# Kernel tuning notes

Hardware: AMD Instinct MI355X
Metric: run time of the kernel (lower is better)

## Reference

```python
import jax, jax.numpy as jnp
import numpy as np

NF = 64        # feature channels (nf == inter_channels == in_channels)
BURST = 14     # burst_size from Args
H = 128
W = 128
SCALE = 0.02   # weight init scale keeps softmax logits in a sane range


def conv1x1(x, w, b):
    # x: [B,C,H,W], w: [O,C], b: [O]
    return jnp.einsum('bchw,oc->bohw', x, w) + b[None, :, None, None]


def setup_inputs() -> dict:
    key = jax.random.key(0)
    ks = jax.random.split(key, 32)
    inp = {'aligned_fea': jax.random.normal(ks[0], (BURST, NF, H, W), dtype=jnp.float32)}
    names = ['gc', 'thc', 'phc', 'Wc', 'gh', 'thh', 'phh', 'Wh', 'gw', 'thw', 'phw', 'Ww']
    for i, n in enumerate(names):
        inp[n + '_w'] = SCALE * jax.random.normal(ks[1 + 2 * i], (NF, NF), dtype=jnp.float32)
        inp[n + '_b'] = SCALE * jax.random.normal(ks[2 + 2 * i], (NF,), dtype=jnp.float32)
    inp['fus_w'] = SCALE * jax.random.normal(ks[26], (NF, BURST * NF * 3), dtype=jnp.float32)
    inp['fus_b'] = SCALE * jax.random.normal(ks[27], (NF,), dtype=jnp.float32)
    return inp


def _forward(aligned_fea,
             gc_w, gc_b, thc_w, thc_b, phc_w, phc_b, Wc_w, Wc_b,
             gh_w, gh_b, thh_w, thh_b, phh_w, phh_b, Wh_w, Wh_b,
             gw_w, gw_b, thw_w, thw_b, phw_w, phw_b, Ww_w, Ww_b,
             fus_w, fus_b):
    B, C, h, w = aligned_fea.shape  # [14, 64, 128, 128]
    x = aligned_fea
    ref = aligned_fea[0:1]  # [1,C,H,W]

    # ---- channel non-local (self) ----
    g = conv1x1(x, gc_w, gc_b).reshape(B, C, h * w)
    th = conv1x1(x, thc_w, thc_b).reshape(B, C, h * w)
    ph = conv1x1(x, phc_w, phc_b).reshape(B, C, h * w)
    f = jnp.einsum('bcn,bdn->bcd', th, ph)            # [B,C,C]
    f = jax.nn.softmax(f, axis=1)                     # softmax over dim=1 as in torch
    y = jnp.einsum('bcd,bdn->bcn', f, g)              # [B,C,HW]
    y = jnp.transpose(y, (0, 2, 1)).reshape(B, C, h, w)  # permute+view as in torch
    zc = conv1x1(y, Wc_w, Wc_b) + x

    # ---- height non-local (cross with ref) ----
    g = conv1x1(x, gh_w, gh_b).reshape(B, h, C * w)
    th = conv1x1(ref, thh_w, thh_b).reshape(1, h, C * w)
    ph = conv1x1(x, phh_w, phh_b).reshape(B, h, C * w)
    f = jnp.einsum('bik,bjk->bij', jnp.broadcast_to(th, (B, h, C * w)), ph)  # [B,H,H]
    f = jax.nn.softmax(f, axis=1)
    y = jnp.einsum('bij,bjk->bik', f, g)              # [B,H,C*W]
    y = jnp.transpose(y, (0, 2, 1)).reshape(B, C, h, w)  # requires H == W
    zh = conv1x1(y, Wh_w, Wh_b) + x

    # ---- width non-local (cross with ref) ----
    g = conv1x1(x, gw_w, gw_b).reshape(B, w, C * h)
    th = conv1x1(ref, thw_w, thw_b).reshape(1, w, C * h)
    ph = conv1x1(x, phw_w, phw_b).reshape(B, w, C * h)
    f = jnp.einsum('bik,bjk->bij', jnp.broadcast_to(th, (B, w, C * h)), ph)  # [B,W,W]
    f = jax.nn.softmax(f, axis=1)
    y = jnp.einsum('bij,bjk->bik', f, g)              # [B,W,C*H]
    y = jnp.transpose(y, (0, 2, 1)).reshape(B, C, h, w)
    zw = conv1x1(y, Ww_w, Ww_b) + x

    # ---- fusion: cat frames along channel in order [c, h, w] ----
    feat = jnp.concatenate([zc.reshape(1, B * C, h, w),
                            zh.reshape(1, B * C, h, w),
                            zw.reshape(1, B * C, h, w)], axis=1)  # [1, 3*B*C, H, W]
    out = conv1x1(feat, fus_w, fus_b)
    return jnp.where(out >= 0, out, 0.2 * out)  # LeakyReLU(0.2)


def reference(aligned_fea,
              gc_w, gc_b, thc_w, thc_b, phc_w, phc_b, Wc_w, Wc_b,
              gh_w, gh_b, thh_w, thh_b, phh_w, phh_b, Wh_w, Wh_b,
              gw_w, gw_b, thw_w, thw_b, phw_w, phw_b, Ww_w, Ww_b,
              fus_w, fus_b):
    return _forward(aligned_fea,
                    gc_w, gc_b, thc_w, thc_b, phc_w, phc_b, Wc_w, Wc_b,
                    gh_w, gh_b, thh_w, thh_b, phh_w, phh_b, Wh_w, Wh_b,
                    gw_w, gw_b, thw_w, thw_b, phw_w, phw_b, Ww_w, Ww_b,
                    fus_w, fus_b)
```

## Files before the change

kernel.cpp:

```cpp
#include <hip/hip_runtime.h>

#define NF 64
#define BURST 14
#define NPIX 16384
#define CN (NF * NPIX)
#define LP 72

typedef short bf16x8 __attribute__((ext_vector_type(8)));
typedef float f32x4 __attribute__((ext_vector_type(4)));
typedef unsigned short us4 __attribute__((ext_vector_type(4)));

__device__ inline unsigned short f2bf(float f) {
    unsigned int u = __float_as_uint(f);
    return (unsigned short)((u + 0x7fffu + ((u >> 16) & 1u)) >> 16);
}
__device__ inline float bf2f(unsigned short u) {
    return __uint_as_float(((unsigned int)u) << 16);
}

__global__ __launch_bounds__(256) void cast_x(const float* __restrict__ X,
                                              unsigned short* __restrict__ XB,
                                              unsigned short* __restrict__ XT,
                                              float* __restrict__ S)
{
    __shared__ unsigned short Xs[128][LP];
    __shared__ float red[256];
    const int tid = threadIdx.x;
    const int p0 = blockIdx.x * 128;
    const int b = blockIdx.y;
    const size_t boff = (size_t)b * CN;
#pragma unroll
    for (int i = 0; i < 8; ++i) {
        const int id = tid + 256 * i;
        const int c = id >> 5, p4 = (id & 31) * 4;
        float4 v = *(const float4*)&X[boff + (size_t)c * NPIX + p0 + p4];
        us4 r;
        r.x = f2bf(v.x); r.y = f2bf(v.y); r.z = f2bf(v.z); r.w = f2bf(v.w);
        *(us4*)&XB[boff + (size_t)c * NPIX + p0 + p4] = r;
        Xs[p4 + 0][c] = r.x; Xs[p4 + 1][c] = r.y;
        Xs[p4 + 2][c] = r.z; Xs[p4 + 3][c] = r.w;
    }
    __syncthreads();
#pragma unroll
    for (int i = 0; i < 4; ++i) {
        const int id = tid + 256 * i;
        const int row = id >> 3, c8 = (id & 7) * 8;
        *(bf16x8*)&XT[boff + (size_t)(p0 + row) * 64 + c8] = *(const bf16x8*)&Xs[row][c8];
    }
    {
        const int c = tid & 63, qq = tid >> 6;
        float sv = 0.f;
        for (int pp = qq * 32; pp < qq * 32 + 32; ++pp) sv += bf2f(Xs[pp][c]);
        red[tid] = sv;
        __syncthreads();
        if (tid < 64) {
            const float t = red[tid] + red[64 + tid] + red[128 + tid] + red[192 + tid];
            atomicAdd(&S[(b * 2 + (p0 >= 8192 ? 1 : 0)) * 64 + tid], t);
        }
    }
}

__global__ __launch_bounds__(256) void precompute(
    const float* __restrict__ fus_w, const float* __restrict__ fus_b,
    const float* __restrict__ Wc, const float* __restrict__ bWc,
    const float* __restrict__ Wh, const float* __restrict__ bWh,
    const float* __restrict__ Ww, const float* __restrict__ bWw,
    const float* __restrict__ gcw, const float* __restrict__ ghw,
    const float* __restrict__ gww,
    unsigned short* __restrict__ M16, unsigned short* __restrict__ Wc16,
    float* __restrict__ cb, unsigned short* __restrict__ gT16)
{
    const int blk = blockIdx.x, tid = threadIdx.x;
    if (blk < 42) {
        __shared__ float Fl[64][65];
        __shared__ float Wl[64][65];
        const int g = blk / 14, b = blk % 14;
        const float* Wg = (g == 0) ? Wc : (g == 1) ? Wh : Ww;
#pragma unroll
        for (int i = 0; i < 4; ++i) {
            const int id = tid + 256 * i;
            const int r = id >> 4, c4 = (id & 15) * 4;
            float4 v = *(const float4*)&fus_w[r * 2688 + g * 896 + b * 64 + c4];
            Fl[r][c4] = v.x; Fl[r][c4 + 1] = v.y; Fl[r][c4 + 2] = v.z; Fl[r][c4 + 3] = v.w;
            float4 u = *(const float4*)&Wg[r * 64 + c4];
            Wl[r][c4] = u.x; Wl[r][c4 + 1] = u.y; Wl[r][c4 + 2] = u.z; Wl[r][c4 + 3] = u.w;
        }
        __syncthreads();
        const int o = tid & 63, qq = tid >> 6;
        float s[16];
#pragma unroll
        for (int i = 0; i < 16; ++i) s[i] = 0.f;
        for (int c2 = 0; c2 < 64; ++c2) {
            const float fv = Fl[o][c2];
#pragma unroll
            for (int i = 0; i < 16; ++i) s[i] += fv * Wl[c2][qq * 16 + i];
        }
        unsigned short* Mout = M16 + (size_t)blk * 4096;
#pragma unroll
        for (int i = 0; i < 16; i += 4) {
            us4 r4; r4.x = f2bf(s[i]); r4.y = f2bf(s[i + 1]); r4.z = f2bf(s[i + 2]); r4.w = f2bf(s[i + 3]);
            *(us4*)&Mout[o * 64 + qq * 16 + i] = r4;
        }
    } else if (blk < 98) {
        const int e0 = (blk - 42) * 1024 + tid * 4;
        const int o = e0 / 896, bc = e0 - o * 896;
        float4 a = *(const float4*)&fus_w[o * 2688 + bc];
        float4 b2 = *(const float4*)&fus_w[o * 2688 + 896 + bc];
        float4 c3 = *(const float4*)&fus_w[o * 2688 + 1792 + bc];
        us4 r;
        r.x = f2bf(a.x + b2.x + c3.x); r.y = f2bf(a.y + b2.y + c3.y);
        r.z = f2bf(a.z + b2.z + c3.z); r.w = f2bf(a.w + b2.w + c3.w);
        *(us4*)&Wc16[e0] = r;
    } else if (blk < 106) {
        __shared__ float red[256];
        const int o = (blk - 98) * 8 + (tid >> 5);
        const int lane = tid & 31;
        float s = 0.f;
        for (int t = 0; t < 84; ++t) {
            const int ch = lane + 32 * t;
            const int g = ch / 896, c2 = ch & 63;
            const float bg = (g == 0) ? bWc[c2] : (g == 1) ? bWh[c2] : bWw[c2];
            s += fus_w[o * 2688 + ch] * bg;
        }
        red[tid] = s;
        __syncthreads();
        if (tid < 8) {
            const int oo = (blk - 98) * 8 + tid;
            float t = fus_b[oo];
            for (int i = 0; i < 32; ++i) t += red[tid * 32 + i];
            cb[oo] = t;
        }
    } else {
        const int g = blk - 106;
        const float* wg = (g == 0) ? gcw : (g == 1) ? ghw : gww;
        unsigned short* dst = gT16 + (size_t)g * 4096;
        for (int e = tid; e < 4096; e += 256) {
            const int cp = e >> 6, d = e & 63;
            dst[e] = f2bf(wg[d * 64 + cp]);
        }
    }
}

__global__ __launch_bounds__(256) void gram(
    const unsigned short* __restrict__ XB, float* __restrict__ Gpart)
{
    const int tid = threadIdx.x;
    const int w = tid >> 6, l = tid & 63, lm = l & 15, q = l >> 4;
    const int b = blockIdx.y;
    const int mo = (w & 1) * 32, no = (w >> 1) * 32;
    const unsigned short* P = XB;
    const unsigned short* Q = XB + (size_t)b * CN;
    f32x4 a0[2][2] = {}, a1[2][2] = {}, a2[2][2] = {}, a3[2][2] = {}, a4[2][2] = {};
#pragma unroll 2
    for (int ki = 0; ki < 8; ++ki) {
        const int k = blockIdx.x * 256 + ki * 32 + q * 8;
        bf16x8 p0[2], p1[2], qm0[2], qm1[2], qn0[2], qn1[2];
#pragma unroll
        for (int mi = 0; mi < 2; ++mi) {
            const size_t rm = (size_t)(mo + mi * 16 + lm) * NPIX;
            const size_t rn = (size_t)(no + mi * 16 + lm) * NPIX;
            p0[mi]  = *(const bf16x8*)&P[rm + k];
            p1[mi]  = *(const bf16x8*)&P[rm + 8192 + k];
            qm0[mi] = *(const bf16x8*)&Q[rm + k];
            qm1[mi] = *(const bf16x8*)&Q[rm + 8192 + k];
            qn0[mi] = *(const bf16x8*)&Q[rn + k];
            qn1[mi] = *(const bf16x8*)&Q[rn + 8192 + k];
        }
#pragma unroll
        for (int mi = 0; mi < 2; ++mi)
#pragma unroll
            for (int ni = 0; ni < 2; ++ni) {
                a0[mi][ni] = __builtin_amdgcn_mfma_f32_16x16x32_bf16(qm0[mi], qn0[ni], a0[mi][ni], 0, 0, 0);
                a0[mi][ni] = __builtin_amdgcn_mfma_f32_16x16x32_bf16(qm1[mi], qn1[ni], a0[mi][ni], 0, 0, 0);
                a1[mi][ni] = __builtin_amdgcn_mfma_f32_16x16x32_bf16(p0[mi], qn0[ni], a1[mi][ni], 0, 0, 0);
                a2[mi][ni] = __builtin_amdgcn_mfma_f32_16x16x32_bf16(p0[mi], qn1[ni], a2[mi][ni], 0, 0, 0);
                a3[mi][ni] = __builtin_amdgcn_mfma_f32_16x16x32_bf16(p1[mi], qn0[ni], a3[mi][ni], 0, 0, 0);
                a4[mi][ni] = __builtin_amdgcn_mfma_f32_16x16x32_bf16(p1[mi], qn1[ni], a4[mi][ni], 0, 0, 0);
            }
    }
    float* Gp = Gpart + (size_t)(blockIdx.x * 14 + b) * 5 * 4096;
#define STORE_Z(zidx, ACC)                                                     \
    for (int mi = 0; mi < 2; ++mi)                                             \
        for (int r = 0; r < 4; ++r)                                            \
            for (int ni = 0; ni < 2; ++ni)                                     \
                Gp[zidx * 4096 + (mo + mi * 16 + q * 4 + r) * 64 + no + ni * 16 + lm] = ACC[mi][ni][r];
    STORE_Z(0, a0) STORE_Z(1, a1) STORE_Z(2, a2) STORE_Z(3, a3) STORE_Z(4, a4)
#undef STORE_Z
}

__global__ __launch_bounds__(256) void gram_reduce(
    const float* __restrict__ Gpart, float* __restrict__ G)
{
    const int e = blockIdx.x * 256 + threadIdx.x;
    float s = 0.f;
#pragma unroll
    for (int ks = 0; ks < 32; ++ks) s += Gpart[(size_t)ks * 286720 + e];
    G[e] = s;
}

__global__ __launch_bounds__(256) void sandwich(
    const float* __restrict__ thc_w, const float* __restrict__ phc_w,
    const float* __restrict__ thc_b, const float* __restrict__ phc_b,
    const float* __restrict__ thh_w, const float* __restrict__ phh_w,
    const float* __restrict__ thh_b, const float* __restrict__ phh_b,
    const float* __restrict__ thw_w, const float* __restrict__ phw_w,
    const float* __restrict__ thw_b, const float* __restrict__ phw_b,
    const float* __restrict__ G, const float* __restrict__ S,
    float* __restrict__ f1, float* __restrict__ f2)
{
    __shared__ float Wt[64][65], Wp[64][65], Gl[64][65], Tl[64][65];
    __shared__ float sth[64], sph[64], uu[64], vv[64], btl[64], bpl[64];
    const int b = blockIdx.x, y = blockIdx.y, tid = threadIdx.x;
    const float *Wth_g, *Wph_g, *bth_g, *bph_g, *Gp;
    float* outp; int dl = 0, dp = 0; float Kn;
    if (y == 0) {
        Wth_g = thc_w; Wph_g = phc_w; bth_g = thc_b; bph_g = phc_b;
        Gp = G + (size_t)(b * 5) * 4096; Kn = 16384.f;
        outp = f1 + (size_t)b * 4096;
    } else {
        const int part = (y - 1) / 4, e = (y - 1) & 3;
        dl = e >> 1; dp = e & 1;
        if (part == 0) { Wth_g = thh_w; Wph_g = phh_w; bth_g = thh_b; bph_g = phh_b; }
        else           { Wth_g = thw_w; Wph_g = phw_w; bth_g = thw_b; bph_g = phw_b; }
        Gp = G + (size_t)(b * 5 + 1 + e) * 4096; Kn = 8192.f;
        outp = f2 + (size_t)(part * 14 + b) * 16384;
    }
#pragma unroll
    for (int i = 0; i < 4; ++i) {
        const int id = tid + 256 * i;
        const int r = id >> 4, c4 = (id & 15) * 4;
        float4 v = *(const float4*)&Wth_g[r * 64 + c4];
        Wt[r][c4] = v.x; Wt[r][c4 + 1] = v.y; Wt[r][c4 + 2] = v.z; Wt[r][c4 + 3] = v.w;
        float4 u = *(const float4*)&Wph_g[r * 64 + c4];
        Wp[r][c4] = u.x; Wp[r][c4 + 1] = u.y; Wp[r][c4 + 2] = u.z; Wp[r][c4 + 3] = u.w;
        float4 g = *(const float4*)&Gp[r * 64 + c4];
        Gl[r][c4] = g.x; Gl[r][c4 + 1] = g.y; Gl[r][c4 + 2] = g.z; Gl[r][c4 + 3] = g.w;
    }
    if (tid < 64) {
        if (y == 0) { const float sf = S[b * 128 + tid] + S[b * 128 + 64 + tid]; sth[tid] = sf; sph[tid] = sf; }
        else { sth[tid] = S[dl * 64 + tid]; sph[tid] = S[b * 128 + dp * 64 + tid]; }
        btl[tid] = bth_g[tid]; bpl[tid] = bph_g[tid];
    }
    __syncthreads();
    if (tid < 64) {
        float su = 0.f, sv = 0.f;
        for (int c = 0; c < 64; ++c) { su += Wt[tid][c] * sth[c]; sv += Wp[tid][c] * sph[c]; }
        uu[tid] = su; vv[tid] = sv;
    }
    const int t = tid & 63, qq = tid >> 6;
    float r16[16];
#pragma unroll
    for (int i = 0; i < 16; ++i) r16[i] = 0.f;
    for (int c = 0; c < 64; ++c) {
        const float fv = Wt[t][c];
#pragma unroll
        for (int i = 0; i < 16; ++i) r16[i] += fv * Gl[c][qq * 16 + i];
    }
#pragma unroll
    for (int i = 0; i < 16; ++i) Tl[t][qq * 16 + i] = r16[i];
    __syncthreads();
#pragma unroll
    for (int i = 0; i < 16; ++i) r16[i] = 0.f;
    for (int c = 0; c < 64; ++c) {
        const float tv = Tl[t][c];
#pragma unroll
        for (int i = 0; i < 16; ++i) r16[i] += tv * Wp[qq * 16 + i][c];
    }
    if (y == 0) {
#pragma unroll
        for (int i = 0; i < 16; ++i) {
            const int d = qq * 16 + i;
            outp[t * 64 + d] = r16[i] + uu[t] * bpl[d] + btl[t] * vv[d] + Kn * btl[t] * bpl[d];
        }
    } else {
#pragma unroll
        for (int i = 0; i < 16; ++i) {
            const int tp = qq * 16 + i;
            outp[(2 * t + dl) * 128 + 2 * tp + dp] =
                r16[i] + uu[t] * bpl[tp] + btl[t] * vv[tp] + Kn * btl[t] * bpl[tp];
        }
    }
}

__global__ __launch_bounds__(256) void softmax_all(
    const float* __restrict__ f1, const float* __restrict__ f2,
    const float* __restrict__ gcb, const float* __restrict__ ghb,
    const float* __restrict__ gwb,
    unsigned short* __restrict__ o1, unsigned short* __restrict__ o2d,
    float* __restrict__ B1, float* __restrict__ B2)
{
    __shared__ float red[256];
    __shared__ float mxA[128], invA[128];
    __shared__ float bgl[64];
    const int bx = blockIdx.x, tid = threadIdx.x;
    if (bx < 14) {
        const float* Fb = f1 + (size_t)bx * 4096;
        unsigned short* Ob = o1 + (size_t)bx * 4096;
        if (tid < 64) bgl[tid] = gcb[tid];
        const int d = tid & 63, qq = tid >> 6;
        float mx = -1e30f;
        for (int c = qq * 16; c < qq * 16 + 16; ++c) mx = fmaxf(mx, Fb[c * 64 + d]);
        red[tid] = mx;
        __syncthreads();
        if (tid < 64) mxA[tid] = fmaxf(fmaxf(red[tid], red[64 + tid]), fmaxf(red[128 + tid], red[192 + tid]));
        __syncthreads();
        const float m = mxA[d];
        float s = 0.f;
        for (int c = qq * 16; c < qq * 16 + 16; ++c) s += __expf(Fb[c * 64 + d] - m);
        red[tid] = s;
        __syncthreads();
        if (tid < 64) invA[tid] = 1.f / (red[tid] + red[64 + tid] + red[128 + tid] + red[192 + tid]);
        __syncthreads();
        const int e0 = tid * 16;
        const int d0 = e0 & 63;
        float bp = 0.f;
#pragma unroll
        for (int i = 0; i < 16; i += 4) {
            us4 r4;
            float v0 = __expf(Fb[e0 + i] - mxA[d0 + i]) * invA[d0 + i];
            float v1 = __expf(Fb[e0 + i + 1] - mxA[d0 + i + 1]) * invA[d0 + i + 1];
            float v2 = __expf(Fb[e0 + i + 2] - mxA[d0 + i + 2]) * invA[d0 + i + 2];
            float v3 = __expf(Fb[e0 + i + 3] - mxA[d0 + i + 3]) * invA[d0 + i + 3];
            bp += v0 * bgl[d0 + i] + v1 * bgl[d0 + i + 1] + v2 * bgl[d0 + i + 2] + v3 * bgl[d0 + i + 3];
            r4.x = f2bf(v0); r4.y = f2bf(v1); r4.z = f2bf(v2); r4.w = f2bf(v3);
            *(us4*)&Ob[e0 + i] = r4;
        }
        red[tid] = bp;
        __syncthreads();
        if (tid < 64)
            B1[bx * 64 + tid] = red[tid * 4] + red[tid * 4 + 1] + red[tid * 4 + 2] + red[tid * 4 + 3];
    } else {
        const int idx = bx - 14;
        const float* Fb = f2 + (size_t)idx * 16384;
        if (tid < 64) bgl[tid] = (idx < 14) ? ghb[tid] : gwb[tid];
        const int j = tid & 127, ih = tid >> 7;
        float mx = -1e30f;
        for (int i = ih * 64; i < ih * 64 + 64; ++i) mx = fmaxf(mx, Fb[i * 128 + j]);
        red[tid] = mx;
        __syncthreads();
        if (tid < 128) mxA[tid] = fmaxf(red[tid], red[128 + tid]);
        __syncthreads();
        const float m = mxA[j];
        float s = 0.f;
        for (int i = ih * 64; i < ih * 64 + 64; ++i) s += __expf(Fb[i * 128 + j] - m);
        red[tid] = s;
        __syncthreads();
        if (tid < 128) invA[tid] = 1.f / (red[tid] + red[128 + tid]);
        __syncthreads();
        const int e0 = tid * 64;
        const int irow = tid >> 1;
        const int j0 = e0 & 127;
        unsigned short vt[2][32];
        float bp = 0.f;
        for (int ii = 0; ii < 64; ++ii) {
            const int jj = j0 + ii;
            const float v = __expf(Fb[e0 + ii] - mxA[jj]) * invA[jj];
            bp += v * bgl[jj >> 1];
            vt[jj & 1][ii >> 1] = f2bf(v);
        }
        unsigned short* Od = o2d + (size_t)idx * 16384 + irow * 64 + (j0 >> 1);
#pragma unroll
        for (int dlt = 0; dlt < 2; ++dlt)
#pragma unroll
            for (int ss = 0; ss < 32; ss += 4)
                *(us4*)&Od[dlt * 8192 + ss] = *(us4*)&vt[dlt][ss];
        red[tid] = bp;
        __syncthreads();
        if (tid < 128) B2[idx * 128 + tid] = red[2 * tid] + red[2 * tid + 1];
    }
}

__global__ __launch_bounds__(256) void kmat(
    const unsigned short* __restrict__ f16_1, const unsigned short* __restrict__ f2d,
    const unsigned short* __restrict__ gT16,
    unsigned short* __restrict__ K1, unsigned short* __restrict__ K2)
{
    const int b = blockIdx.x, y = blockIdx.y, tid = threadIdx.x;
    const int w = tid >> 6, l = tid & 63, lm = l & 15, q = l >> 4;
    if (y == 0) {
        const unsigned short* A = f16_1 + (size_t)b * 4096;
        const unsigned short* Bm = gT16;
        const int mo = (w & 1) * 32, no = (w >> 1) * 32;
        f32x4 acc[2][2] = {};
#pragma unroll
        for (int ks = 0; ks < 2; ++ks) {
            const int k = ks * 32 + q * 8;
            bf16x8 a[2], bb[2];
#pragma unroll
            for (int mi = 0; mi < 2; ++mi) a[mi] = *(const bf16x8*)&A[(mo + mi * 16 + lm) * 64 + k];
#pragma unroll
            for (int ni = 0; ni < 2; ++ni) bb[ni] = *(const bf16x8*)&Bm[(no + ni * 16 + lm) * 64 + k];
#pragma unroll
            for (int mi = 0; mi < 2; ++mi)
#pragma unroll
                for (int ni = 0; ni < 2; ++ni)
                    acc[mi][ni] = __builtin_amdgcn_mfma_f32_16x16x32_bf16(a[mi], bb[ni], acc[mi][ni], 0, 0, 0);
        }
        unsigned short* Kp = K1 + (size_t)b * 4096;
#pragma unroll
        for (int mi = 0; mi < 2; ++mi)
#pragma unroll
            for (int r = 0; r < 4; ++r)
#pragma unroll
                for (int ni = 0; ni < 2; ++ni)
                    Kp[(mo + mi * 16 + q * 4 + r) * 64 + no + ni * 16 + lm] = f2bf(acc[mi][ni][r]);
    } else {
        const int part = y - 1;
        const unsigned short* Bm = gT16 + (size_t)(1 + part) * 4096;
        unsigned short* Kp = K2 + (size_t)(part * 14 + b) * 16384;
        for (int dlt = 0; dlt < 2; ++dlt) {
            const unsigned short* A = f2d + (size_t)(part * 14 + b) * 16384 + dlt * 8192;
            const int mo = (w & 1) * 64, no = (w >> 1) * 32;
            f32x4 acc[4][2] = {};
#pragma unroll
            for (int ks = 0; ks < 2; ++ks) {
                const int k = ks * 32 + q * 8;
                bf16x8 a[4], bb[2];
#pragma unroll
                for (int mi = 0; mi < 4; ++mi) a[mi] = *(const bf16x8*)&A[(mo + mi * 16 + lm) * 64 + k];
#pragma unroll
                for (int ni = 0; ni < 2; ++ni) bb[ni] = *(const bf16x8*)&Bm[(no + ni * 16 + lm) * 64 + k];
#pragma unroll
                for (int mi = 0; mi < 4; ++mi)
#pragma unroll
                    for (int ni = 0; ni < 2; ++ni)
                        acc[mi][ni] = __builtin_amdgcn_mfma_f32_16x16x32_bf16(a[mi], bb[ni], acc[mi][ni], 0, 0, 0);
            }
#pragma unroll
            for (int mi = 0; mi < 4; ++mi)
#pragma unroll
                for (int r = 0; r < 4; ++r)
#pragma unroll
                    for (int ni = 0; ni < 2; ++ni)
                        Kp[dlt * 8192 + (mo + mi * 16 + q * 4 + r) * 64 + no + ni * 16 + lm] = f2bf(acc[mi][ni][r]);
        }
    }
}

__global__ __launch_bounds__(256) void fold_res(
    const unsigned short* __restrict__ Wcomb, const unsigned short* __restrict__ XT,
    float* __restrict__ Out)
{
    const int tid = threadIdx.x;
    const int w = tid >> 6, l = tid & 63, lm = l & 15, q = l >> 4;
    const int p0 = blockIdx.x * 64 + (w >> 1) * 32;
    const int oh = (w & 1) * 32;
    f32x4 acc[2][2] = {};
    for (int b = 0; b < 14; ++b) {
#pragma unroll
        for (int ks = 0; ks < 2; ++ks) {
            const int c0 = ks * 32 + q * 8;
            bf16x8 a[2], bb[2];
#pragma unroll
            for (int mi = 0; mi < 2; ++mi)
                a[mi] = *(const bf16x8*)&Wcomb[(oh + mi * 16 + lm) * 896 + b * 64 + c0];
#pragma unroll
            for (int ni = 0; ni < 2; ++ni)
                bb[ni] = *(const bf16x8*)&XT[(size_t)b * CN + (size_t)(p0 + ni * 16 + lm) * 64 + c0];
#pragma unroll
            for (int mi = 0; mi < 2; ++mi)
#pragma unroll
                for (int ni = 0; ni < 2; ++ni)
                    acc[mi][ni] = __builtin_amdgcn_mfma_f32_16x16x32_bf16(a[mi], bb[ni], acc[mi][ni], 0, 0, 0);
        }
    }
#pragma unroll
    for (int mi = 0; mi < 2; ++mi)
#pragma unroll
        for (int r = 0; r < 4; ++r) {
            const int o = oh + mi * 16 + q * 4 + r;
#pragma unroll
            for (int ni = 0; ni < 2; ++ni)
                Out[(size_t)o * NPIX + p0 + ni * 16 + lm] = acc[mi][ni][r];
        }
}

__global__ __launch_bounds__(256) void pv1k(
    const unsigned short* __restrict__ XT, const unsigned short* __restrict__ K1,
    const float* __restrict__ B1, unsigned short* __restrict__ Y)
{
    const int tid = threadIdx.x;
    const int w = tid >> 6, l = tid & 63, lm = l & 15, q = l >> 4;
    const int b = blockIdx.z;
    const int p0 = blockIdx.x * 256 + w * 64;
    const unsigned short* Xb = XT + (size_t)b * CN;
    const unsigned short* Kb = K1 + (size_t)b * 4096;
    f32x4 acc[4][4] = {};
#pragma unroll
    for (int ks = 0; ks < 2; ++ks) {
        const int c0 = ks * 32 + q * 8;
        bf16x8 a[4], bb[4];
#pragma unroll
        for (int mi = 0; mi < 4; ++mi) a[mi] = *(const bf16x8*)&Xb[(size_t)(p0 + mi * 16 + lm) * 64 + c0];
#pragma unroll
        for (int ni = 0; ni < 4; ++ni) bb[ni] = *(const bf16x8*)&Kb[(ni * 16 + lm) * 64 + c0];
#pragma unroll
        for (int mi = 0; mi < 4; ++mi)
#pragma unroll
            for (int ni = 0; ni < 4; ++ni)
                acc[mi][ni] = __builtin_amdgcn_mfma_f32_16x16x32_bf16(a[mi], bb[ni], acc[mi][ni], 0, 0, 0);
    }
    unsigned short* Yb = Y + (size_t)b * CN;
#pragma unroll
    for (int mi = 0; mi < 4; ++mi)
#pragma unroll
        for (int r = 0; r < 4; ++r) {
            const int p = p0 + mi * 16 + q * 4 + r;
#pragma unroll
            for (int ni = 0; ni < 4; ++ni) {
                const int c = ni * 16 + lm;
                Yb[(size_t)p * 64 + c] = f2bf(acc[mi][ni][r] + B1[b * 64 + c]);
            }
        }
}

__global__ __launch_bounds__(256) void pv23k(
    const unsigned short* __restrict__ XT, const unsigned short* __restrict__ K2,
    const float* __restrict__ B2, unsigned short* __restrict__ Y2,
    unsigned short* __restrict__ Y3)
{
    const int tid = threadIdx.x;
    const int w = tid >> 6, l = tid & 63, lm = l & 15, q = l >> 4;
    const int part = blockIdx.z / 14, b = blockIdx.z % 14;
    const int k00 = blockIdx.x * 256 + w * 64;
    const int i0 = blockIdx.y * 64;
    const unsigned short* Xb = XT + (size_t)b * CN;
    const unsigned short* Kb = K2 + (size_t)(part * 14 + b) * 16384;
    const float* Bb = B2 + (part * 14 + b) * 128;
    f32x4 acc[4][4] = {};
#pragma unroll
    for (int dlt = 0; dlt < 2; ++dlt) {
#pragma unroll
        for (int ks = 0; ks < 2; ++ks) {
            const int c0 = ks * 32 + q * 8;
            bf16x8 a[4], bb[4];
#pragma unroll
            for (int mi = 0; mi < 4; ++mi)
                a[mi] = *(const bf16x8*)&Xb[(size_t)(dlt * 8192 + k00 + mi * 16 + lm) * 64 + c0];
#pragma unroll
            for (int ni = 0; ni < 4; ++ni)
                bb[ni] = *(const bf16x8*)&Kb[dlt * 8192 + (i0 + ni * 16 + lm) * 64 + c0];
#pragma unroll
            for (int mi = 0; mi < 4; ++mi)
#pragma unroll
                for (int ni = 0; ni < 4; ++ni)
                    acc[mi][ni] = __builtin_amdgcn_mfma_f32_16x16x32_bf16(a[mi], bb[ni], acc[mi][ni], 0, 0, 0);
        }
    }
    unsigned short* Yb = (part ? Y3 : Y2) + (size_t)b * CN;
#pragma unroll
    for (int mi = 0; mi < 4; ++mi)
#pragma unroll
        for (int r = 0; r < 4; ++r) {
            const int k = k00 + mi * 16 + q * 4 + r;
#pragma unroll
            for (int ni = 0; ni < 4; ++ni) {
                const int ii = i0 + ni * 16 + lm;
                Yb[(size_t)k * 128 + ii] = f2bf(acc[mi][ni][r] + Bb[ii]);
            }
        }
}

__global__ __launch_bounds__(256) void yfold(
    const unsigned short* __restrict__ M16,
    const unsigned short* __restrict__ Y1, const unsigned short* __restrict__ Y2,
    const unsigned short* __restrict__ Y3, float* __restrict__ Out)
{
    __shared__ unsigned short As[64][LP];
    __shared__ unsigned short Ss[128][LP];
    const int tid = threadIdx.x;
    const int z = blockIdx.z;
    const unsigned short* Ap = M16 + (size_t)z * 14 * 4096;
    const unsigned short* S = (z == 0) ? Y1 : (z == 1) ? Y2 : Y3;
    const int p0 = blockIdx.x * 128;
    const int t0 = blockIdx.y * 7;
    const int w = tid >> 6, l = tid & 63, lm = l & 15, q = l >> 4;
    const int mo = (w & 1) * 32;
    const int no = (w >> 1) * 64;
    f32x4 acc[2][4] = {};

    for (int t = t0; t < t0 + 7; ++t) {
        __syncthreads();
#pragma unroll
        for (int i = 0; i < 2; ++i) {
            const int ch = tid + 256 * i;
            const int row = ch >> 3, c8 = (ch & 7) * 8;
            *(bf16x8*)&As[row][c8] = *(const bf16x8*)&Ap[(size_t)t * 4096 + (size_t)row * 64 + c8];
        }
#pragma unroll
        for (int i = 0; i < 4; ++i) {
            const int id = tid + 256 * i;
            const int c = id & 63, p8 = (id >> 6) * 8;
            bf16x8 v = *(const bf16x8*)&S[(size_t)t * CN + (size_t)c * NPIX + p0 + p8];
#pragma unroll
            for (int j = 0; j < 8; ++j) Ss[p8 + j][c] = (unsigned short)v[j];
        }
        __syncthreads();
#pragma unroll
        for (int ks = 0; ks < 2; ++ks) {
            const int c0 = ks * 32 + q * 8;
            bf16x8 a[2], bb[4];
#pragma unroll
            for (int mi = 0; mi < 2; ++mi) a[mi] = *(const bf16x8*)&As[mo + mi * 16 + lm][c0];
#pragma unroll
            for (int ni = 0; ni < 4; ++ni) bb[ni] = *(const bf16x8*)&Ss[no + ni * 16 + lm][c0];
#pragma unroll
            for (int mi = 0; mi < 2; ++mi)
#pragma unroll
                for (int ni = 0; ni < 4; ++ni)
                    acc[mi][ni] = __builtin_amdgcn_mfma_f32_16x16x32_bf16(a[mi], bb[ni], acc[mi][ni], 0, 0, 0);
        }
    }
#pragma unroll
    for (int mi = 0; mi < 2; ++mi)
#pragma unroll
        for (int r = 0; r < 4; ++r) {
            const int o = mo + mi * 16 + q * 4 + r;
#pragma unroll
            for (int ni = 0; ni < 4; ++ni)
                atomicAdd(&Out[(size_t)o * NPIX + p0 + no + ni * 16 + lm], acc[mi][ni][r]);
        }
}

__global__ __launch_bounds__(256) void leaky_cb(float* __restrict__ O, const float* __restrict__ cb)
{
    const int i = blockIdx.x * 256 + threadIdx.x;
    float4 v = ((float4*)O)[i];
    const float b = cb[(i * 4) >> 14];
    v.x += b; v.y += b; v.z += b; v.w += b;
    v.x = v.x >= 0.f ? v.x : 0.2f * v.x;
    v.y = v.y >= 0.f ? v.y : 0.2f * v.y;
    v.z = v.z >= 0.f ? v.z : 0.2f * v.z;
    v.w = v.w >= 0.f ? v.w : 0.2f * v.w;
    ((float4*)O)[i] = v;
}

extern "C" void kernel_launch(void* const* d_in, const int* in_sizes, int n_in,
                              void* d_out, int out_size, void* d_ws, size_t ws_size,
                              hipStream_t stream)
{
    const float* x     = (const float*)d_in[0];
    const float* gc_w  = (const float*)d_in[1];
    const float* gc_b  = (const float*)d_in[2];
    const float* thc_w = (const float*)d_in[3];
    const float* thc_b = (const float*)d_in[4];
    const float* phc_w = (const float*)d_in[5];
    const float* phc_b = (const float*)d_in[6];
    const float* Wc_w  = (const float*)d_in[7];
    const float* Wc_b  = (const float*)d_in[8];
    const float* gh_w  = (const float*)d_in[9];
    const float* gh_b  = (const float*)d_in[10];
    const float* thh_w = (const float*)d_in[11];
    const float* thh_b = (const float*)d_in[12];
    const float* phh_w = (const float*)d_in[13];
    const float* phh_b = (const float*)d_in[14];
    const float* Wh_w  = (const float*)d_in[15];
    const float* Wh_b  = (const float*)d_in[16];
    const float* gw_w  = (const float*)d_in[17];
    const float* gw_b  = (const float*)d_in[18];
    const float* thw_w = (const float*)d_in[19];
    const float* thw_b = (const float*)d_in[20];
    const float* phw_w = (const float*)d_in[21];
    const float* phw_b = (const float*)d_in[22];
    const float* Ww_w  = (const float*)d_in[23];
    const float* Ww_b  = (const float*)d_in[24];
    const float* fus_w = (const float*)d_in[25];
    const float* fus_b = (const float*)d_in[26];

    float* out = (float*)d_out;

    char* p = (char*)d_ws;
    unsigned short* xb   = (unsigned short*)p; p += (size_t)BURST * CN * 2;
    unsigned short* xT   = (unsigned short*)p; p += (size_t)BURST * CN * 2;
    unsigned short* y1   = (unsigned short*)p; p += (size_t)BURST * CN * 2;
    unsigned short* y2   = (unsigned short*)p; p += (size_t)BURST * CN * 2;
    unsigned short* y3   = (unsigned short*)p; p += (size_t)BURST * CN * 2;
    float*          Gbuf = (float*)p;          p += (size_t)BURST * 5 * 4096 * 4;
    float*          sbuf = (float*)p;          p += (size_t)BURST * 2 * 64 * 4;
    float*          f1b  = (float*)p;          p += (size_t)BURST * 4096 * 4;
    float*          f2b  = (float*)p;          p += (size_t)2 * BURST * 16384 * 4;
    unsigned short* f16_1 = (unsigned short*)p; p += (size_t)BURST * 4096 * 2;
    unsigned short* f2d  = (unsigned short*)p; p += (size_t)2 * BURST * 16384 * 2;
    unsigned short* K1   = (unsigned short*)p; p += (size_t)BURST * 4096 * 2;
    unsigned short* K2   = (unsigned short*)p; p += (size_t)2 * BURST * 16384 * 2;
    float*          B1   = (float*)p;          p += (size_t)BURST * 64 * 4;
    float*          B2   = (float*)p;          p += (size_t)2 * BURST * 128 * 4;
    unsigned short* M16  = (unsigned short*)p; p += (size_t)42 * 4096 * 2;
    unsigned short* Wc16 = (unsigned short*)p; p += (size_t)64 * 896 * 2;
    unsigned short* gT16 = (unsigned short*)p; p += (size_t)3 * 4096 * 2;
    float*          cbv  = (float*)p;          p += 256;

    float* Gpart = (float*)y1;

    hipMemsetAsync(sbuf, 0, (size_t)BURST * 2 * 64 * 4, stream);

    cast_x<<<dim3(128, 14), 256, 0, stream>>>(x, xb, xT, sbuf);
    precompute<<<109, 256, 0, stream>>>(fus_w, fus_b, Wc_w, Wc_b, Wh_w, Wh_b, Ww_w, Ww_b,
                                        gc_w, gh_w, gw_w, M16, Wc16, cbv, gT16);
    gram<<<dim3(32, 14), 256, 0, stream>>>(xb, Gpart);
    gram_reduce<<<1120, 256, 0, stream>>>(Gpart, Gbuf);
    sandwich<<<dim3(14, 9), 256, 0, stream>>>(
        thc_w, phc_w, thc_b, phc_b, thh_w, phh_w, thh_b, phh_b,
        thw_w, phw_w, thw_b, phw_b, Gbuf, sbuf, f1b, f2b);
    softmax_all<<<42, 256, 0, stream>>>(f1b, f2b, gc_b, gh_b, gw_b,
                                        f16_1, f2d, B1, B2);
    kmat<<<dim3(14, 3), 256, 0, stream>>>(f16_1, f2d, gT16, K1, K2);
    fold_res<<<256, 256, 0, stream>>>(Wc16, xT, out);
    pv1k<<<dim3(64, 1, BURST), 256, 0, stream>>>(xT, K1, B1, y1);
    pv23k<<<dim3(32, 2, 2 * BURST), 256, 0, stream>>>(xT, K2, B2, y2, y3);
    yfold<<<dim3(128, 2, 3), 256, 0, stream>>>(M16, y1, y2, y3, out);
    leaky_cb<<<1024, 256, 0, stream>>>(out, cbv);
}
```

Measured before the change: 331.0 us.

## Fuse residual fold, PV products and Y fold into one kernel via LDS staging

Replaces four kernels (fold_res, pv1k, pv23k, yfold) with a single pvfold kernel. Each block computes its per-frame Y tiles (channel, height and width attention products) into double-buffered shared memory and immediately contracts them with the fusion weights, accumulating into the output. This removes the write and re-read of three large bf16 Y intermediates through global memory and three kernel launches. In exchange the output needs a memset plus atomic adds from two frame-half blocks, more syncthreads per frame, and only 512 blocks with small tiles and strided XT gathers.

Result: slower. 341.2 us (+3.1%).

```diff
diff --git a/kernel.cpp b/kernel.cpp
--- a/kernel.cpp
+++ b/kernel.cpp
@@ -437,188 +437,168 @@
     }
 }
 
-__global__ __launch_bounds__(256) void fold_res(
-    const unsigned short* __restrict__ Wcomb, const unsigned short* __restrict__ XT,
-    float* __restrict__ Out)
-{
-    const int tid = threadIdx.x;
-    const int w = tid >> 6, l = tid & 63, lm = l & 15, q = l >> 4;
-    const int p0 = blockIdx.x * 64 + (w >> 1) * 32;
-    const int oh = (w & 1) * 32;
+__device__ __forceinline__ void s1_p1(
+    const unsigned short* __restrict__ XT, const unsigned short* __restrict__ K1,
+    const float* __restrict__ B1, int b, int h1,
+    int mo, int no, int lm, int q, unsigned short (*Yb)[LP])
+{
     f32x4 acc[2][2] = {};
-    for (int b = 0; b < 14; ++b) {
+    const unsigned short* Xb = XT + (size_t)b * CN;
+    const unsigned short* Kb = K1 + (size_t)b * 4096;
+#pragma unroll
+    for (int ks = 0; ks < 2; ++ks) {
+        const int c0 = ks * 32 + q * 8;
+        bf16x8 a[2], bb[2];
+#pragma unroll
+        for (int mi = 0; mi < 2; ++mi)
+            a[mi] = *(const bf16x8*)&Xb[((size_t)(mo + mi * 16 + lm) * 256 + h1) * 64 + c0];
+#pragma unroll
+        for (int ni = 0; ni < 2; ++ni)
+            bb[ni] = *(const bf16x8*)&Kb[(no + ni * 16 + lm) * 64 + c0];
+#pragma unroll
+        for (int mi = 0; mi < 2; ++mi)
+#pragma unroll
+            for (int ni = 0; ni < 2; ++ni)
+                acc[mi][ni] = __builtin_amdgcn_mfma_f32_16x16x32_bf16(a[mi], bb[ni], acc[mi][ni], 0, 0, 0);
+    }
+#pragma unroll
+    for (int mi = 0; mi < 2; ++mi)
+#pragma unroll
+        for (int r = 0; r < 4; ++r) {
+            const int c2 = mo + mi * 16 + q * 4 + r;
+#pragma unroll
+            for (int ni = 0; ni < 2; ++ni) {
+                const int c = no + ni * 16 + lm;
+                Yb[c][c2] = f2bf(acc[mi][ni][r] + B1[b * 64 + c]);
+            }
+        }
+}
+
+__device__ __forceinline__ void s1_p23(
+    const unsigned short* __restrict__ XT, const unsigned short* __restrict__ K2,
+    const float* __restrict__ B2, int part, int b, int h2, int i0,
+    int mo, int no, int lm, int q, unsigned short (*Yb)[LP])
+{
+    f32x4 acc[2][2] = {};
+    const unsigned short* Xb = XT + (size_t)b * CN;
+    const unsigned short* Kb = K2 + (size_t)(part * 14 + b) * 16384;
+    const float* Bb = B2 + (part * 14 + b) * 128;
+#pragma unroll
+    for (int dlt = 0; dlt < 2; ++dlt)
 #pragma unroll
         for (int ks = 0; ks < 2; ++ks) {
             const int c0 = ks * 32 + q * 8;
             bf16x8 a[2], bb[2];
 #pragma unroll
             for (int mi = 0; mi < 2; ++mi)
-                a[mi] = *(const bf16x8*)&Wcomb[(oh + mi * 16 + lm) * 896 + b * 64 + c0];
+                a[mi] = *(const bf16x8*)&Xb[((size_t)dlt * 8192 + (size_t)(mo + mi * 16 + lm) * 128 + h2) * 64 + c0];
 #pragma unroll
             for (int ni = 0; ni < 2; ++ni)
-                bb[ni] = *(const bf16x8*)&XT[(size_t)b * CN + (size_t)(p0 + ni * 16 + lm) * 64 + c0];
+                bb[ni] = *(const bf16x8*)&Kb[dlt * 8192 + (i0 + no + ni * 16 + lm) * 64 + c0];
 #pragma unroll
             for (int mi = 0; mi < 2; ++mi)
 #pragma unroll
                 for (int ni = 0; ni < 2; ++ni)
                     acc[mi][ni] = __builtin_amdgcn_mfma_f32_16x16x32_bf16(a[mi], bb[ni], acc[mi][ni], 0, 0, 0);
         }
-    }
 #pragma unroll
     for (int mi = 0; mi < 2; ++mi)
 #pragma unroll
         for (int r = 0; r < 4; ++r) {
-            const int o = oh + mi * 16 + q * 4 + r;
+            const int c2 = mo + mi * 16 + q * 4 + r;
+#pragma unroll
+            for (int ni = 0; ni < 2; ++ni) {
+                const int iiL = no + ni * 16 + lm;
+                Yb[iiL][c2] = f2bf(acc[mi][ni][r] + Bb[i0 + iiL]);
+            }
+        }
+}
+
+__device__ __forceinline__ void s2(
+    const unsigned short* __restrict__ M16, int z, int b,
+    int mo, int no, int lm, int q, const unsigned short (*Yb)[LP],
+    f32x4 (*oacc)[2])
+{
+    const unsigned short* Mp = M16 + (size_t)(z * 14 + b) * 4096;
+#pragma unroll
+    for (int ks = 0; ks < 2; ++ks) {
+        const int c0 = ks * 32 + q * 8;
+        bf16x8 a[2], bb[2];
+#pragma unroll
+        for (int mi = 0; mi < 2; ++mi)
+            a[mi] = *(const bf16x8*)&Mp[(mo + mi * 16 + lm) * 64 + c0];
+#pragma unroll
+        for (int ni = 0; ni < 2; ++ni)
+            bb[ni] = *(const bf16x8*)&Yb[no + ni * 16 + lm][c0];
+#pragma unroll
+        for (int mi = 0; mi < 2; ++mi)
 #pragma unroll
             for (int ni = 0; ni < 2; ++ni)
-                Out[(size_t)o * NPIX + p0 + ni * 16 + lm] = acc[mi][ni][r];
-        }
-}
-
-__global__ __launch_bounds__(256) void pv1k(
-    const unsigned short* __restrict__ XT, const unsigned short* __restrict__ K1,
-    const float* __restrict__ B1, unsigned short* __restrict__ Y)
-{
+                oacc[mi][ni] = __builtin_amdgcn_mfma_f32_16x16x32_bf16(a[mi], bb[ni], oacc[mi][ni], 0, 0, 0);
+    }
+}
+
+__global__ __launch_bounds__(256) void pvfold(
+    const unsigned short* __restrict__ XT,
+    const unsigned short* __restrict__ K1, const float* __restrict__ B1,
+    const unsigned short* __restrict__ K2, const float* __restrict__ B2,
+    const unsigned short* __restrict__ M16,
+    const unsigned short* __restrict__ Wcomb,
+    float* __restrict__ Out)
+{
+    __shared__ unsigned short Ys[2][64][LP];
     const int tid = threadIdx.x;
     const int w = tid >> 6, l = tid & 63, lm = l & 15, q = l >> 4;
-    const int b = blockIdx.z;
-    const int p0 = blockIdx.x * 256 + w * 64;
-    const unsigned short* Xb = XT + (size_t)b * CN;
-    const unsigned short* Kb = K1 + (size_t)b * 4096;
-    f32x4 acc[4][4] = {};
-#pragma unroll
-    for (int ks = 0; ks < 2; ++ks) {
-        const int c0 = ks * 32 + q * 8;
-        bf16x8 a[4], bb[4];
-#pragma unroll
-        for (int mi = 0; mi < 4; ++mi) a[mi] = *(const bf16x8*)&Xb[(size_t)(p0 + mi * 16 + lm) * 64 + c0];
-#pragma unroll
-        for (int ni = 0; ni < 4; ++ni) bb[ni] = *(const bf16x8*)&Kb[(ni * 16 + lm) * 64 + c0];
-#pragma unroll
-        for (int mi = 0; mi < 4; ++mi)
-#pragma unroll
-            for (int ni = 0; ni < 4; ++ni)
-                acc[mi][ni] = __builtin_amdgcn_mfma_f32_16x16x32_bf16(a[mi], bb[ni], acc[mi][ni], 0, 0, 0);
-    }
-    unsigned short* Yb = Y + (size_t)b * CN;
-#pragma unroll
-    for (int mi = 0; mi < 4; ++mi)
-#pragma unroll
-        for (int r = 0; r < 4; ++r) {
-            const int p = p0 + mi * 16 + q * 4 + r;
-#pragma unroll
-            for (int ni = 0; ni < 4; ++ni) {
-                const int c = ni * 16 + lm;
-                Yb[(size_t)p * 64 + c] = f2bf(acc[mi][ni][r] + B1[b * 64 + c]);
-            }
-        }
-}
-
-__global__ __launch_bounds__(256) void pv23k(
-    const unsigned short* __restrict__ XT, const unsigned short* __restrict__ K2,
-    const float* __restrict__ B2, unsigned short* __restrict__ Y2,
-    unsigned short* __restrict__ Y3)
-{
-    const int tid = threadIdx.x;
-    const int w = tid >> 6, l = tid & 63, lm = l & 15, q = l >> 4;
-    const int part = blockIdx.z / 14, b = blockIdx.z % 14;
-    const int k00 = blockIdx.x * 256 + w * 64;
-    const int i0 = blockIdx.y * 64;
-    const unsigned short* Xb = XT + (size_t)b * CN;
-    const unsigned short* Kb = K2 + (size_t)(part * 14 + b) * 16384;
-    const float* Bb = B2 + (part * 14 + b) * 128;
-    f32x4 acc[4][4] = {};
-#pragma unroll
-    for (int dlt = 0; dlt < 2; ++dlt) {
+    const int P0 = blockIdx.x * 64;
+    const int h1 = blockIdx.x;
+    const int h2 = blockIdx.x >> 1;
+    const int i0 = (blockIdx.x & 1) * 64;
+    const int b0 = blockIdx.y * 7;
+    const int mo = (w & 1) * 32, no = (w >> 1) * 32;
+    f32x4 oacc[2][2] = {};
+
+    for (int b = b0; b < b0 + 7; ++b) {
 #pragma unroll
         for (int ks = 0; ks < 2; ++ks) {
             const int c0 = ks * 32 + q * 8;
-            bf16x8 a[4], bb[4];
-#pragma unroll
-            for (int mi = 0; mi < 4; ++mi)
-                a[mi] = *(const bf16x8*)&Xb[(size_t)(dlt * 8192 + k00 + mi * 16 + lm) * 64 + c0];
-#pragma unroll
-            for (int ni = 0; ni < 4; ++ni)
-                bb[ni] = *(const bf16x8*)&Kb[dlt * 8192 + (i0 + ni * 16 + lm) * 64 + c0];
-#pragma unroll
-            for (int mi = 0; mi < 4; ++mi)
-#pragma unroll
-                for (int ni = 0; ni < 4; ++ni)
-                    acc[mi][ni] = __builtin_amdgcn_mfma_f32_16x16x32_bf16(a[mi], bb[ni], acc[mi][ni], 0, 0, 0);
-        }
-    }
-    unsigned short* Yb = (part ? Y3 : Y2) + (size_t)b * CN;
-#pragma unroll
-    for (int mi = 0; mi < 4; ++mi)
-#pragma unroll
-        for (int r = 0; r < 4; ++r) {
-            const int k = k00 + mi * 16 + q * 4 + r;
-#pragma unroll
-            for (int ni = 0; ni < 4; ++ni) {
-                const int ii = i0 + ni * 16 + lm;
-                Yb[(size_t)k * 128 + ii] = f2bf(acc[mi][ni][r] + Bb[ii]);
-            }
-        }
-}
-
-__global__ __launch_bounds__(256) void yfold(
-    const unsigned short* __restrict__ M16,
-    const unsigned short* __restrict__ Y1, const unsigned short* __restrict__ Y2,
-    const unsigned short* __restrict__ Y3, float* __restrict__ Out)
-{
-    __shared__ unsigned short As[64][LP];
-    __shared__ unsigned short Ss[128][LP];
-    const int tid = threadIdx.x;
-    const int z = blockIdx.z;
-    const unsigned short* Ap = M16 + (size_t)z * 14 * 4096;
-    const unsigned short* S = (z == 0) ? Y1 : (z == 1) ? Y2 : Y3;
-    const int p0 = blockIdx.x * 128;
-    const int t0 = blockIdx.y * 7;
-    const int w = tid >> 6, l = tid & 63, lm = l & 15, q = l >> 4;
-    const int mo = (w & 1) * 32;
-    const int no = (w >> 1) * 64;
-    f32x4 acc[2][4] = {};
-
-    for (int t = t0; t < t0 + 7; ++t) {
-        __syncthreads();
-#pragma unroll
-        for (int i = 0; i < 2; ++i) {
-            const int ch = tid + 256 * i;
-            const int row = ch >> 3, c8 = (ch & 7) * 8;
-            *(bf16x8*)&As[row][c8] = *(const bf16x8*)&Ap[(size_t)t * 4096 + (size_t)row * 64 + c8];
-        }
-#pragma unroll
-        for (int i = 0; i < 4; ++i) {
-            const int id = tid + 256 * i;
-            const int c = id & 63, p8 = (id >> 6) * 8;
-            bf16x8 v = *(const bf16x8*)&S[(size_t)t * CN + (size_t)c * NPIX + p0 + p8];
-#pragma unroll
-            for (int j = 0; j < 8; ++j) Ss[p8 + j][c] = (unsigned short)v[j];
-        }
-        __syncthreads();
-#pragma unroll
-        for (int ks = 0; ks < 2; ++ks) {
-            const int c0 = ks * 32 + q * 8;
-            bf16x8 a[2], bb[4];
-#pragma unroll
-            for (int mi = 0; mi < 2; ++mi) a[mi] = *(const bf16x8*)&As[mo + mi * 16 + lm][c0];
-#pragma unroll
-            for (int ni = 0; ni < 4; ++ni) bb[ni] = *(const bf16x8*)&Ss[no + ni * 16 + lm][c0];
+            bf16x8 a[2], bb[2];
 #pragma unroll
             for (int mi = 0; mi < 2; ++mi)
-#pragma unroll
-                for (int ni = 0; ni < 4; ++ni)
-                    acc[mi][ni] = __builtin_amdgcn_mfma_f32_16x16x32_bf16(a[mi], bb[ni], acc[mi][ni], 0, 0, 0);
-        }
-    }
+                a[mi] = *(const bf16x8*)&Wcomb[(mo + mi * 16 + lm) * 896 + b * 64 + c0];
+#pragma unroll
+            for (int ni = 0; ni < 2; ++ni)
+                bb[ni] = *(const bf16x8*)&XT[(size_t)b * CN + (size_t)(P0 + no + ni * 16 + lm) * 64 + c0];
+#pragma unroll
+            for (int mi = 0; mi < 2; ++mi)
+#pragma unroll
+                for (int ni = 0; ni < 2; ++ni)
+                    oacc[mi][ni] = __builtin_amdgcn_mfma_f32_16x16x32_bf16(a[mi], bb[ni], oacc[mi][ni], 0, 0, 0);
+        }
+    }
+
+    int cur = 0;
+    s1_p1(XT, K1, B1, b0, h1, mo, no, lm, q, Ys[0]);
+    for (int b = b0; b < b0 + 7; ++b) {
+        __syncthreads();
+        s2(M16, 0, b, mo, no, lm, q, (const unsigned short (*)[LP])Ys[cur], oacc);
+        s1_p23(XT, K2, B2, 0, b, h2, i0, mo, no, lm, q, Ys[cur ^ 1]);
+        __syncthreads();
+        s2(M16, 1, b, mo, no, lm, q, (const unsigned short (*)[LP])Ys[cur ^ 1], oacc);
+        s1_p23(XT, K2, B2, 1, b, h2, i0, mo, no, lm, q, Ys[cur]);
+        __syncthreads();
+        s2(M16, 2, b, mo, no, lm, q, (const unsigned short (*)[LP])Ys[cur], oacc);
+        if (b + 1 < b0 + 7) s1_p1(XT, K1, B1, b + 1, h1, mo, no, lm, q, Ys[cur ^ 1]);
+        cur ^= 1;
+    }
+
 #pragma unroll
     for (int mi = 0; mi < 2; ++mi)
 #pragma unroll
         for (int r = 0; r < 4; ++r) {
             const int o = mo + mi * 16 + q * 4 + r;
 #pragma unroll
-            for (int ni = 0; ni < 4; ++ni)
-                atomicAdd(&Out[(size_t)o * NPIX + p0 + no + ni * 16 + lm], acc[mi][ni][r]);
+            for (int ni = 0; ni < 2; ++ni)
+                atomicAdd(&Out[(size_t)o * NPIX + P0 + no + ni * 16 + lm], oacc[mi][ni][r]);
         }
 }
 
@@ -672,9 +652,7 @@
     char* p = (char*)d_ws;
     unsigned short* xb   = (unsigned short*)p; p += (size_t)BURST * CN * 2;
     unsigned short* xT   = (unsigned short*)p; p += (size_t)BURST * CN * 2;
-    unsigned short* y1   = (unsigned short*)p; p += (size_t)BURST * CN * 2;
-    unsigned short* y2   = (unsigned short*)p; p += (size_t)BURST * CN * 2;
-    unsigned short* y3   = (unsigned short*)p; p += (size_t)BURST * CN * 2;
+    float*          Gpart = (float*)p;         p += (size_t)32 * 286720 * 4;
     float*          Gbuf = (float*)p;          p += (size_t)BURST * 5 * 4096 * 4;
     float*          sbuf = (float*)p;          p += (size_t)BURST * 2 * 64 * 4;
     float*          f1b  = (float*)p;          p += (size_t)BURST * 4096 * 4;
@@ -690,9 +668,8 @@
     unsigned short* gT16 = (unsigned short*)p; p += (size_t)3 * 4096 * 2;
     float*          cbv  = (float*)p;          p += 256;
 
-    float* Gpart = (float*)y1;
-
     hipMemsetAsync(sbuf, 0, (size_t)BURST * 2 * 64 * 4, stream);
+    hipMemsetAsync(out, 0, (size_t)NF * NPIX * 4, stream);
 
     cast_x<<<dim3(128, 14), 256, 0, stream>>>(x, xb, xT, sbuf);
     precompute<<<109, 256, 0, stream>>>(fus_w, fus_b, Wc_w, Wc_b, Wh_w, Wh_b, Ww_w, Ww_b,
@@ -705,9 +682,6 @@
     softmax_all<<<42, 256, 0, stream>>>(f1b, f2b, gc_b, gh_b, gw_b,
                                         f16_1, f2d, B1, B2);
     kmat<<<dim3(14, 3), 256, 0, stream>>>(f16_1, f2d, gT16, K1, K2);
-    fold_res<<<256, 256, 0, stream>>>(Wc16, xT, out);
-    pv1k<<<dim3(64, 1, BURST), 256, 0, stream>>>(xT, K1, B1, y1);
-    pv23k<<<dim3(32, 2, 2 * BURST), 256, 0, stream>>>(xT, K2, B2, y2, y3);
-    yfold<<<dim3(128, 2, 3), 256, 0, stream>>>(M16, y1, y2, y3, out);
+    pvfold<<<dim3(256, 2), 256, 0, stream>>>(xT, K1, B1, K2, B2, M16, Wc16, out);
     leaky_cb<<<1024, 256, 0, stream>>>(out, cbv);
 }
```
